# Kernel optimization log

Measured on AMD Instinct MI355X. Metric: run time of the kernel, lower is better.

## Reference

```python
import jax, jax.numpy as jnp
from jax import lax
import numpy as np

VOCAB = 50000
EMBED = 300
H = 128
NUM_CLASS = 2
B, L = 4, 512


def _lstm(x, Wih, Whh, b):
    # x: (B, L, D) -> hidden sequence (B, L, H); PyTorch gate order i,f,g,o
    Bn = x.shape[0]
    h0 = jnp.zeros((Bn, H), dtype=x.dtype)
    c0 = jnp.zeros((Bn, H), dtype=x.dtype)

    def step(carry, xt):
        h, c = carry
        g = xt @ Wih + h @ Whh + b  # (B, 4H)
        i, f, gg, o = jnp.split(g, 4, axis=-1)
        i = jax.nn.sigmoid(i)
        f = jax.nn.sigmoid(f)
        gg = jnp.tanh(gg)
        o = jax.nn.sigmoid(o)
        c = f * c + i * gg
        h = o * jnp.tanh(c)
        return (h, c), h

    _, hs = lax.scan(step, (h0, c0), jnp.swapaxes(x, 0, 1))
    return jnp.swapaxes(hs, 0, 1)


def setup_inputs() -> dict:
    key = jax.random.key(0)
    ks = jax.random.split(key, 12)
    s = lambda fan_in: 1.0 / np.sqrt(fan_in)
    inp = {
        "question_content": jax.random.randint(ks[0], (B, L), 0, VOCAB, dtype=jnp.int32),
        "answer_content": jax.random.randint(ks[1], (B, L), 0, VOCAB, dtype=jnp.int32),
        "embed_table": jax.random.normal(ks[2], (VOCAB, EMBED), dtype=jnp.float32) * 0.1,
        "W_ih": jax.random.uniform(ks[3], (EMBED, 4 * H), jnp.float32, -s(H), s(H)),
        "W_hh": jax.random.uniform(ks[4], (H, 4 * H), jnp.float32, -s(H), s(H)),
        "b_lstm": jax.random.uniform(ks[5], (4 * H,), jnp.float32, -s(H), s(H)),
        "Wa": jax.random.uniform(ks[6], (2 * H, H), jnp.float32, -s(2 * H), s(2 * H)),
        "ba": jnp.zeros((H,), jnp.float32),
        "Wq": jax.random.uniform(ks[7], (2 * H, 1), jnp.float32, -s(2 * H), s(2 * H)),
        "bq": jnp.zeros((1,), jnp.float32),
        "Wans": jax.random.uniform(ks[8], (2 * H, 1), jnp.float32, -s(2 * H), s(2 * H)),
        "bans": jnp.zeros((1,), jnp.float32),
        "Wlast": jax.random.uniform(ks[9], (2 * H, NUM_CLASS), jnp.float32, -s(2 * H), s(2 * H)),
        "blast": jnp.zeros((NUM_CLASS,), jnp.float32),
    }
    return inp


def reference(question_content, answer_content, embed_table, W_ih, W_hh, b_lstm,
              Wa, ba, Wq, bq, Wans, bans, Wlast, blast):
    q_emb = embed_table[question_content]  # (B, Lq, EMBED)
    a_emb = embed_table[answer_content]    # (B, La, EMBED)
    q_lstm = _lstm(q_emb, W_ih, W_hh, b_lstm)  # (B, Lq, H)
    a_lstm = _lstm(a_emb, W_ih, W_hh, b_lstm)  # (B, La, H)

    # A = tanh(Wa @ cat(q_expand, a_expand) + ba); split Wa to avoid the concat copy
    Wa_q, Wa_a = Wa[:H], Wa[H:]
    proj_q = q_lstm @ Wa_q              # (B, Lq, H)
    proj_a = a_lstm @ Wa_a              # (B, La, H)
    A = jnp.tanh(proj_q[:, :, None, :] + proj_a[:, None, :, :] + ba)  # (B, Lq, La, H)

    r_q = jnp.max(A, axis=1)  # max over question positions -> (B, La, H)
    r_a = jnp.max(A, axis=2)  # max over answer positions   -> (B, Lq, H)

    cat_q = jnp.concatenate([q_lstm, r_q], axis=-1)  # (B, L, 2H) (Lq == La)
    cat_a = jnp.concatenate([a_lstm, r_a], axis=-1)
    alpha_q = jax.nn.softmax(cat_q @ Wq + bq, axis=-2)    # (B, L, 1)
    alpha_a = jax.nn.softmax(cat_a @ Wans + bans, axis=-2)

    feature_q = jnp.sum(alpha_q * r_q, axis=-2)  # (B, H)
    feature_a = jnp.sum(alpha_a * r_a, axis=-2)  # (B, H)
    feature_last = jnp.concatenate([feature_q, feature_a], axis=-1)  # (B, 2H)

    score = jax.nn.log_softmax(feature_last @ Wlast + blast, axis=-1)
    predict = jnp.argmax(score, axis=-1)
    return score, predict
```

## Files before the change

### kernel.cpp

```cpp
#include <hip/hip_runtime.h>
#include <hip/hip_bf16.h>

#define EMBED 300
#define HD    128
#define LLEN  512
#define G4    512

#define OFF_LSTM 2097152
#define OFF_PROJ 2621440
#define OFF_MX   3145728

typedef _Float16 half8 __attribute__((ext_vector_type(8)));
typedef float    f32x4 __attribute__((ext_vector_type(4)));

__device__ __forceinline__ float fsig(float x) {
    return __fdividef(1.f, 1.f + __expf(-x));
}
__device__ __forceinline__ float ftanh(float x) {
    return 1.f - __fdividef(2.f, __expf(2.f * x) + 1.f);
}

__global__ __launch_bounds__(256) void k1_gemm(
    const int* __restrict__ qc, const int* __restrict__ ac,
    const float* __restrict__ emb, const float* __restrict__ wih,
    const float* __restrict__ bl, float* __restrict__ preg)
{
    __shared__ float As[32][65];
    __shared__ float Bs[32][64];
    const int m0 = blockIdx.x * 64;
    const int n0 = blockIdx.y * 64;
    const int tid = threadIdx.x;
    const int tx = tid & 15, ty = tid >> 4;
    float acc[4][4] = {};

    for (int k0 = 0; k0 < 300; k0 += 32) {
        #pragma unroll
        for (int i = 0; i < 8; ++i) {
            int e = tid + i * 256;
            int m = e >> 5, kk = e & 31;
            int row = m0 + m;
            int c = row >> 11, b = (row >> 9) & 3, t = row & 511;
            int tok = (c == 0 ? qc : ac)[b * LLEN + t];
            int k = k0 + kk;
            As[kk][m] = (k < 300) ? emb[(size_t)tok * EMBED + k] : 0.f;
        }
        #pragma unroll
        for (int i = 0; i < 8; ++i) {
            int e = tid + i * 256;
            int kk = e >> 6, n = e & 63;
            int k = k0 + kk;
            Bs[kk][n] = (k < 300) ? wih[k * G4 + n0 + n] : 0.f;
        }
        __syncthreads();
        #pragma unroll
        for (int kk = 0; kk < 32; ++kk) {
            float a[4], bv[4];
            #pragma unroll
            for (int i = 0; i < 4; ++i) a[i] = As[kk][ty * 4 + i];
            #pragma unroll
            for (int j = 0; j < 4; ++j) bv[j] = Bs[kk][tx * 4 + j];
            #pragma unroll
            for (int i = 0; i < 4; ++i)
                #pragma unroll
                for (int j = 0; j < 4; ++j)
                    acc[i][j] += a[i] * bv[j];
        }
        __syncthreads();
    }
    #pragma unroll
    for (int i = 0; i < 4; ++i) {
        int row = m0 + ty * 4 + i;
        #pragma unroll
        for (int j = 0; j < 4; ++j) {
            int n = n0 + tx * 4 + j;
            preg[(size_t)row * G4 + n] = acc[i][j] + bl[n];
        }
    }
}

__global__ __launch_bounds__(512, 1) void k2_lstm_mfma(
    const float* __restrict__ whh, const float* __restrict__ preg,
    const float* __restrict__ wa,
    float* __restrict__ lstm, float* __restrict__ proj, float* __restrict__ mx)
{
    const int seq = blockIdx.x;
    const int tid = threadIdx.x;
    const int w  = tid >> 6;
    const int l  = tid & 63;
    const int li = l & 15;
    const int g  = l >> 4;

    __shared__ __align__(16) _Float16 hist[32 * 136];

    half8 afrag[4][4];
    #pragma unroll
    for (int s = 0; s < 4; ++s) {
        const int mg = s * 128 + w * 16 + li;
        #pragma unroll
        for (int kt = 0; kt < 4; ++kt) {
            half8 v;
            #pragma unroll
            for (int e = 0; e < 8; ++e)
                v[e] = (_Float16)whh[(kt * 32 + g * 8 + e) * G4 + mg];
            afrag[kt][s] = v;
        }
    }
    const int s_side = seq >> 2;
    half8 afragW[4];
    #pragma unroll
    for (int kt = 0; kt < 4; ++kt) {
        half8 v;
        #pragma unroll
        for (int e = 0; e < 8; ++e)
            v[e] = (_Float16)wa[(s_side * 128 + kt * 32 + g * 8 + e) * 128 + (w * 16 + li)];
        afragW[kt] = v;
    }

    for (int i = tid; i < 32 * 68; i += 512) ((unsigned*)hist)[i] = 0u;

    const f32x4* pg4 = (const f32x4*)(preg + (size_t)seq * LLEN * G4);
    const int pgo = w * 4 + g;
    const int r   = li & 3;
    const int unit = w * 16 + g * 4 + r;
    const bool wlane = li < 4;
    float* outp = lstm + (size_t)seq * LLEN * HD + unit;
    float cst = 0.f;
    float pmr0 = -1e30f, pmr1 = -1e30f, pmr2 = -1e30f, pmr3 = -1e30f;

    f32x4 pgA[4], pgB[4];
    #pragma unroll
    for (int s = 0; s < 4; ++s) pgA[s] = pg4[0 * 128 + s * 32 + pgo];
    #pragma unroll
    for (int s = 0; s < 4; ++s) pgB[s] = pg4[1 * 128 + s * 32 + pgo];

    __syncthreads();

#define LSTM_STEP(T, PGV, RDS, WRS)                                            \
    {                                                                          \
        half8 bfrag[4];                                                        \
        _Pragma("unroll")                                                      \
        for (int kt = 0; kt < 4; ++kt)                                         \
            bfrag[kt] = *(const half8*)(hist + (RDS) * 136 + kt * 32 + g * 8); \
        f32x4 a0 = PGV[0], a1 = PGV[1], a2 = PGV[2], a3 = PGV[3];              \
        {                                                                      \
            int tp = (T) + 2; if (tp > 511) tp = 511;                          \
            _Pragma("unroll")                                                  \
            for (int s = 0; s < 4; ++s) PGV[s] = pg4[tp * 128 + s * 32 + pgo]; \
        }                                                                      \
        _Pragma("unroll")                                                      \
        for (int kt = 0; kt < 4; ++kt) {                                       \
            a0 = __builtin_amdgcn_mfma_f32_16x16x32_f16(afrag[kt][0], bfrag[kt], a0, 0, 0, 0); \
            a1 = __builtin_amdgcn_mfma_f32_16x16x32_f16(afrag[kt][1], bfrag[kt], a1, 0, 0, 0); \
            a2 = __builtin_amdgcn_mfma_f32_16x16x32_f16(afrag[kt][2], bfrag[kt], a2, 0, 0, 0); \
            a3 = __builtin_amdgcn_mfma_f32_16x16x32_f16(afrag[kt][3], bfrag[kt], a3, 0, 0, 0); \
        }                                                                      \
        float xi = (r == 0) ? a0[0] : (r == 1) ? a0[1] : (r == 2) ? a0[2] : a0[3]; \
        float xf = (r == 0) ? a1[0] : (r == 1) ? a1[1] : (r == 2) ? a1[2] : a1[3]; \
        float xg = (r == 0) ? a2[0] : (r == 1) ? a2[1] : (r == 2) ? a2[2] : a2[3]; \
        float xo = (r == 0) ? a3[0] : (r == 1) ? a3[1] : (r == 2) ? a3[2] : a3[3]; \
        float i_ = fsig(xi), f_ = fsig(xf), g_ = ftanh(xg), o_ = fsig(xo);     \
        cst = f_ * cst + i_ * g_;                                              \
        float h = o_ * ftanh(cst);                                             \
        if (wlane) {                                                           \
            outp[(size_t)(T) * HD] = h;                                        \
            hist[(WRS) * 136 + unit] = (_Float16)h;                            \
        }                                                                      \
        asm volatile("s_waitcnt lgkmcnt(0)" ::: "memory");                     \
        __builtin_amdgcn_sched_barrier(0);                                     \
        __builtin_amdgcn_s_barrier();                                          \
        __builtin_amdgcn_sched_barrier(0);                                     \
    }

#define PROJ_BATCH(P, TBASE)                                                   \
    {                                                                          \
        const _Float16* hb = hist + ((P) * 16 + li) * 136 + g * 8;             \
        half8 bb0 = *(const half8*)(hb + 0 * 32);                              \
        half8 bb1 = *(const half8*)(hb + 1 * 32);                              \
        half8 bb2 = *(const half8*)(hb + 2 * 32);                              \
        half8 bb3 = *(const half8*)(hb + 3 * 32);                              \
        f32x4 pa = {0.f, 0.f, 0.f, 0.f};                                       \
        pa = __builtin_amdgcn_mfma_f32_16x16x32_f16(afragW[0], bb0, pa, 0, 0, 0); \
        pa = __builtin_amdgcn_mfma_f32_16x16x32_f16(afragW[1], bb1, pa, 0, 0, 0); \
        pa = __builtin_amdgcn_mfma_f32_16x16x32_f16(afragW[2], bb2, pa, 0, 0, 0); \
        pa = __builtin_amdgcn_mfma_f32_16x16x32_f16(afragW[3], bb3, pa, 0, 0, 0); \
        float* pp = proj + (size_t)seq * LLEN * HD                             \
                  + (size_t)((TBASE) + li) * HD + w * 16 + g * 4;              \
        *(f32x4*)pp = pa;                                                      \
        pmr0 = fmaxf(pmr0, pa[0]);                                             \
        pmr1 = fmaxf(pmr1, pa[1]);                                             \
        pmr2 = fmaxf(pmr2, pa[2]);                                             \
        pmr3 = fmaxf(pmr3, pa[3]);                                             \
    }

    #pragma unroll 1
    for (int tto = 0; tto < 16; ++tto) {
        const int tb = tto * 32;
        #pragma unroll
        for (int u = 0; u < 16; ++u) {
            const int t0 = tb + u * 2;
            LSTM_STEP(t0,     pgA, (2 * u + 31) & 31, 2 * u);
            LSTM_STEP(t0 + 1, pgB, 2 * u, 2 * u + 1);
            if (u == 7)  PROJ_BATCH(0, tb);
            if (u == 15) PROJ_BATCH(1, tb + 16);
        }
    }
#undef LSTM_STEP
#undef PROJ_BATCH

    #pragma unroll
    for (int m = 1; m <= 8; m <<= 1) {
        pmr0 = fmaxf(pmr0, __shfl_xor(pmr0, m, 64));
        pmr1 = fmaxf(pmr1, __shfl_xor(pmr1, m, 64));
        pmr2 = fmaxf(pmr2, __shfl_xor(pmr2, m, 64));
        pmr3 = fmaxf(pmr3, __shfl_xor(pmr3, m, 64));
    }
    if (li == 0) {
        mx[seq * HD + w * 16 + g * 4 + 0] = pmr0;
        mx[seq * HD + w * 16 + g * 4 + 1] = pmr1;
        mx[seq * HD + w * 16 + g * 4 + 2] = pmr2;
        mx[seq * HD + w * 16 + g * 4 + 3] = pmr3;
    }
}

__global__ __launch_bounds__(512) void k45a_attn(
    const float* __restrict__ lstm, const float* __restrict__ proj,
    const float* __restrict__ mx, const float* __restrict__ ba,
    const float* __restrict__ wq, const float* __restrict__ wans,
    float* __restrict__ pn, float* __restrict__ pd)
{
    const int bid = blockIdx.x;
    const int chunk = bid & 3, sb = bid >> 2;
    const int s = sb >> 2, b = sb & 3;
    const int tid = threadIdx.x;
    const int wave = tid >> 6, lane = tid & 63;

    __shared__ float nred[8][128];
    __shared__ float dred[8];

    const float* wv = (s == 0) ? wq : wans;
    const float* lb = lstm + (size_t)sb * LLEN * HD;
    const float* po = proj + (size_t)((1 - s) * 4 + b) * LLEN * HD;

    const float mb1 = mx[sb * HD + lane] + ba[lane];
    const float mb2 = mx[sb * HD + lane + 64] + ba[lane + 64];
    const float wv1a = wv[lane], wv1b = wv[lane + 64];
    const float wv2a = wv[128 + lane], wv2b = wv[192 + lane];

    float n1 = 0.f, n2 = 0.f, den = 0.f;
    #pragma unroll 4
    for (int jj = 0; jj < 16; ++jj) {
        const int j = chunk * 128 + wave + jj * 8;
        float L1 = lb[(size_t)j * HD + lane];
        float L2 = lb[(size_t)j * HD + lane + 64];
        float P1 = po[(size_t)j * HD + lane];
        float P2 = po[(size_t)j * HD + lane + 64];
        float r1 = ftanh(mb1 + P1), r2 = ftanh(mb2 + P2);
        float sc = L1 * wv1a + L2 * wv1b + r1 * wv2a + r2 * wv2b;
        #pragma unroll
        for (int o = 32; o; o >>= 1) sc += __shfl_xor(sc, o, 64);
        float e = __expf(sc);
        den += e;
        n1 += e * r1;
        n2 += e * r2;
    }
    nred[wave][lane] = n1;
    nred[wave][lane + 64] = n2;
    if (lane == 0) dred[wave] = den;
    __syncthreads();

    if (tid < 128) {
        float s8 = 0.f;
        #pragma unroll
        for (int i = 0; i < 8; ++i) s8 += nred[i][tid];
        pn[bid * 128 + tid] = s8;
    }
    if (tid == 128) {
        float dd = 0.f;
        #pragma unroll
        for (int i = 0; i < 8; ++i) dd += dred[i];
        pd[bid] = dd;
    }
}

__global__ __launch_bounds__(256) void k45b_final(
    const float* __restrict__ pn, const float* __restrict__ pd,
    const float* __restrict__ wlast, const float* __restrict__ blast,
    float* __restrict__ outp)
{
    const int b = blockIdx.x;
    const int tid = threadIdx.x;
    __shared__ float feats[2][128];
    __shared__ float cls[256];

    {
        const int ss = tid >> 7, h = tid & 127;
        const int base = (ss * 4 + b) * 4;
        float num = pn[(base + 0) * 128 + h] + pn[(base + 1) * 128 + h]
                  + pn[(base + 2) * 128 + h] + pn[(base + 3) * 128 + h];
        float dd  = pd[base + 0] + pd[base + 1] + pd[base + 2] + pd[base + 3];
        feats[ss][h] = num / dd;
    }
    __syncthreads();

    if (tid < 128) {
        float f0 = feats[0][tid], f1 = feats[1][tid];
        cls[tid]       = f0 * wlast[tid * 2 + 0] + f1 * wlast[(128 + tid) * 2 + 0];
        cls[128 + tid] = f0 * wlast[tid * 2 + 1] + f1 * wlast[(128 + tid) * 2 + 1];
    }
    __syncthreads();
    if (tid < 64) {
        float a0 = cls[tid] + cls[tid + 64];
        float a1 = cls[128 + tid] + cls[192 + tid];
        #pragma unroll
        for (int o = 32; o; o >>= 1) {
            a0 += __shfl_down(a0, o, 64);
            a1 += __shfl_down(a1, o, 64);
        }
        if (tid == 0) {
            float l0 = blast[0] + a0, l1 = blast[1] + a1;
            float mxl = fmaxf(l0, l1);
            float lse = mxl + logf(__expf(l0 - mxl) + __expf(l1 - mxl));
            outp[b * 2 + 0] = l0 - lse;
            outp[b * 2 + 1] = l1 - lse;
            outp[8 + b]     = (l1 > l0) ? 1.f : 0.f;
        }
    }
}

extern "C" void kernel_launch(void* const* d_in, const int* in_sizes, int n_in,
                              void* d_out, int out_size, void* d_ws, size_t ws_size,
                              hipStream_t stream)
{
    const int*   qc    = (const int*)d_in[0];
    const int*   ac    = (const int*)d_in[1];
    const float* emb   = (const float*)d_in[2];
    const float* wih   = (const float*)d_in[3];
    const float* whh   = (const float*)d_in[4];
    const float* bl    = (const float*)d_in[5];
    const float* wa    = (const float*)d_in[6];
    const float* ba    = (const float*)d_in[7];
    const float* wq    = (const float*)d_in[8];
    const float* wans  = (const float*)d_in[10];
    const float* wlast = (const float*)d_in[12];
    const float* blast = (const float*)d_in[13];

    float* ws   = (float*)d_ws;
    float* preg = ws;
    float* lstm = ws + OFF_LSTM;
    float* proj = ws + OFF_PROJ;
    float* mx   = ws + OFF_MX;
    float* pn   = ws;
    float* pd   = ws + 4096;

    k1_gemm<<<dim3(64, 8), 256, 0, stream>>>(qc, ac, emb, wih, bl, preg);
    k2_lstm_mfma<<<8, 512, 0, stream>>>(whh, preg, wa, lstm, proj, mx);
    k45a_attn<<<32, 512, 0, stream>>>(lstm, proj, mx, ba, wq, wans, pn, pd);
    k45b_final<<<4, 256, 0, stream>>>(pn, pd, wlast, blast, (float*)d_out);
}
```

Baseline: 381.6 us.

## Split LSTM recurrent matmul K across two wave groups with LDS reduction

Doubles the LSTM block to 1024 threads and has the upper eight waves compute half of the K-reduction of h@Whh, passing partial sums through shared memory to the lower waves. The lower waves add the partials and apply the gate nonlinearities. This shortens the dependent MFMA chain per timestep. It costs an extra LDS store/load and a second block-wide barrier on every step, and the time loop is no longer fully unrolled.

```diff
diff --git a/kernel.cpp b/kernel.cpp
--- a/kernel.cpp
+++ b/kernel.cpp
@@ -78,31 +78,35 @@
     }
 }
 
-__global__ __launch_bounds__(512, 1) void k2_lstm_mfma(
+__global__ __launch_bounds__(1024, 1) void k2_lstm_mfma(
     const float* __restrict__ whh, const float* __restrict__ preg,
     const float* __restrict__ wa,
     float* __restrict__ lstm, float* __restrict__ proj, float* __restrict__ mx)
 {
     const int seq = blockIdx.x;
     const int tid = threadIdx.x;
-    const int w  = tid >> 6;
+    const int w   = tid >> 6;
+    const int wl  = w & 7;
+    const bool lower = w < 8;
     const int l  = tid & 63;
     const int li = l & 15;
     const int g  = l >> 4;
+    const int ktb = lower ? 0 : 2;
 
     __shared__ __align__(16) _Float16 hist[32 * 136];
-
-    half8 afrag[4][4];
+    __shared__ __align__(16) f32x4 red[4 * 8 * 64];
+
+    half8 afrag[2][4];
     #pragma unroll
     for (int s = 0; s < 4; ++s) {
-        const int mg = s * 128 + w * 16 + li;
-        #pragma unroll
-        for (int kt = 0; kt < 4; ++kt) {
+        const int mg = s * 128 + wl * 16 + li;
+        #pragma unroll
+        for (int ktl = 0; ktl < 2; ++ktl) {
             half8 v;
             #pragma unroll
             for (int e = 0; e < 8; ++e)
-                v[e] = (_Float16)whh[(kt * 32 + g * 8 + e) * G4 + mg];
-            afrag[kt][s] = v;
+                v[e] = (_Float16)whh[((ktb + ktl) * 32 + g * 8 + e) * G4 + mg];
+            afrag[ktl][s] = v;
         }
     }
     const int s_side = seq >> 2;
@@ -112,67 +116,84 @@
         half8 v;
         #pragma unroll
         for (int e = 0; e < 8; ++e)
-            v[e] = (_Float16)wa[(s_side * 128 + kt * 32 + g * 8 + e) * 128 + (w * 16 + li)];
+            v[e] = (_Float16)wa[(s_side * 128 + kt * 32 + g * 8 + e) * 128 + (wl * 16 + li)];
         afragW[kt] = v;
     }
 
-    for (int i = tid; i < 32 * 68; i += 512) ((unsigned*)hist)[i] = 0u;
+    for (int i = tid; i < 32 * 68; i += 1024) ((unsigned*)hist)[i] = 0u;
 
     const f32x4* pg4 = (const f32x4*)(preg + (size_t)seq * LLEN * G4);
-    const int pgo = w * 4 + g;
+    const int pgo = wl * 4 + g;
     const int r   = li & 3;
-    const int unit = w * 16 + g * 4 + r;
+    const int unit = wl * 16 + g * 4 + r;
     const bool wlane = li < 4;
     float* outp = lstm + (size_t)seq * LLEN * HD + unit;
     float cst = 0.f;
     float pmr0 = -1e30f, pmr1 = -1e30f, pmr2 = -1e30f, pmr3 = -1e30f;
 
-    f32x4 pgA[4], pgB[4];
-    #pragma unroll
-    for (int s = 0; s < 4; ++s) pgA[s] = pg4[0 * 128 + s * 32 + pgo];
-    #pragma unroll
-    for (int s = 0; s < 4; ++s) pgB[s] = pg4[1 * 128 + s * 32 + pgo];
+    f32x4 pgA[4] = {}, pgB[4] = {};
+    if (lower) {
+        #pragma unroll
+        for (int s = 0; s < 4; ++s) pgA[s] = pg4[0 * 128 + s * 32 + pgo];
+        #pragma unroll
+        for (int s = 0; s < 4; ++s) pgB[s] = pg4[1 * 128 + s * 32 + pgo];
+    }
 
     __syncthreads();
 
 #define LSTM_STEP(T, PGV, RDS, WRS)                                            \
     {                                                                          \
-        half8 bfrag[4];                                                        \
-        _Pragma("unroll")                                                      \
-        for (int kt = 0; kt < 4; ++kt)                                         \
-            bfrag[kt] = *(const half8*)(hist + (RDS) * 136 + kt * 32 + g * 8); \
-        f32x4 a0 = PGV[0], a1 = PGV[1], a2 = PGV[2], a3 = PGV[3];              \
-        {                                                                      \
+        const _Float16* hp = hist + (RDS) * 136 + ktb * 32 + g * 8;            \
+        half8 bfrag0 = *(const half8*)(hp);                                    \
+        half8 bfrag1 = *(const half8*)(hp + 32);                               \
+        f32x4 a0, a1, a2, a3;                                                  \
+        if (lower) {                                                           \
+            a0 = PGV[0]; a1 = PGV[1]; a2 = PGV[2]; a3 = PGV[3];                \
             int tp = (T) + 2; if (tp > 511) tp = 511;                          \
             _Pragma("unroll")                                                  \
             for (int s = 0; s < 4; ++s) PGV[s] = pg4[tp * 128 + s * 32 + pgo]; \
+        } else {                                                               \
+            a0 = (f32x4){0.f,0.f,0.f,0.f}; a1 = a0; a2 = a0; a3 = a0;          \
         }                                                                      \
-        _Pragma("unroll")                                                      \
-        for (int kt = 0; kt < 4; ++kt) {                                       \
-            a0 = __builtin_amdgcn_mfma_f32_16x16x32_f16(afrag[kt][0], bfrag[kt], a0, 0, 0, 0); \
-            a1 = __builtin_amdgcn_mfma_f32_16x16x32_f16(afrag[kt][1], bfrag[kt], a1, 0, 0, 0); \
-            a2 = __builtin_amdgcn_mfma_f32_16x16x32_f16(afrag[kt][2], bfrag[kt], a2, 0, 0, 0); \
-            a3 = __builtin_amdgcn_mfma_f32_16x16x32_f16(afrag[kt][3], bfrag[kt], a3, 0, 0, 0); \
-        }                                                                      \
-        float xi = (r == 0) ? a0[0] : (r == 1) ? a0[1] : (r == 2) ? a0[2] : a0[3]; \
-        float xf = (r == 0) ? a1[0] : (r == 1) ? a1[1] : (r == 2) ? a1[2] : a1[3]; \
-        float xg = (r == 0) ? a2[0] : (r == 1) ? a2[1] : (r == 2) ? a2[2] : a2[3]; \
-        float xo = (r == 0) ? a3[0] : (r == 1) ? a3[1] : (r == 2) ? a3[2] : a3[3]; \
-        float i_ = fsig(xi), f_ = fsig(xf), g_ = ftanh(xg), o_ = fsig(xo);     \
-        cst = f_ * cst + i_ * g_;                                              \
-        float h = o_ * ftanh(cst);                                             \
-        if (wlane) {                                                           \
-            outp[(size_t)(T) * HD] = h;                                        \
-            hist[(WRS) * 136 + unit] = (_Float16)h;                            \
+        a0 = __builtin_amdgcn_mfma_f32_16x16x32_f16(afrag[0][0], bfrag0, a0, 0, 0, 0); \
+        a1 = __builtin_amdgcn_mfma_f32_16x16x32_f16(afrag[0][1], bfrag0, a1, 0, 0, 0); \
+        a2 = __builtin_amdgcn_mfma_f32_16x16x32_f16(afrag[0][2], bfrag0, a2, 0, 0, 0); \
+        a3 = __builtin_amdgcn_mfma_f32_16x16x32_f16(afrag[0][3], bfrag0, a3, 0, 0, 0); \
+        a0 = __builtin_amdgcn_mfma_f32_16x16x32_f16(afrag[1][0], bfrag1, a0, 0, 0, 0); \
+        a1 = __builtin_amdgcn_mfma_f32_16x16x32_f16(afrag[1][1], bfrag1, a1, 0, 0, 0); \
+        a2 = __builtin_amdgcn_mfma_f32_16x16x32_f16(afrag[1][2], bfrag1, a2, 0, 0, 0); \
+        a3 = __builtin_amdgcn_mfma_f32_16x16x32_f16(afrag[1][3], bfrag1, a3, 0, 0, 0); \
+        if (!lower) {                                                          \
+            f32x4* rp = red + wl * 64 + l;                                     \
+            rp[0] = a0; rp[512] = a1; rp[1024] = a2; rp[1536] = a3;            \
         }                                                                      \
         asm volatile("s_waitcnt lgkmcnt(0)" ::: "memory");                     \
         __builtin_amdgcn_sched_barrier(0);                                     \
         __builtin_amdgcn_s_barrier();                                          \
         __builtin_amdgcn_sched_barrier(0);                                     \
+        if (lower) {                                                           \
+            const f32x4* rp = red + wl * 64 + l;                               \
+            a0 += rp[0]; a1 += rp[512]; a2 += rp[1024]; a3 += rp[1536];        \
+            float xi = (r == 0) ? a0[0] : (r == 1) ? a0[1] : (r == 2) ? a0[2] : a0[3]; \
+            float xf = (r == 0) ? a1[0] : (r == 1) ? a1[1] : (r == 2) ? a1[2] : a1[3]; \
+            float xg = (r == 0) ? a2[0] : (r == 1) ? a2[1] : (r == 2) ? a2[2] : a2[3]; \
+            float xo = (r == 0) ? a3[0] : (r == 1) ? a3[1] : (r == 2) ? a3[2] : a3[3]; \
+            float i_ = fsig(xi), f_ = fsig(xf), g_ = ftanh(xg), o_ = fsig(xo); \
+            cst = f_ * cst + i_ * g_;                                          \
+            float h = o_ * ftanh(cst);                                         \
+            if (wlane) {                                                       \
+                outp[(size_t)(T) * HD] = h;                                    \
+                hist[(WRS) * 136 + unit] = (_Float16)h;                        \
+            }                                                                  \
+        }                                                                      \
+        asm volatile("s_waitcnt lgkmcnt(0)" ::: "memory");                     \
+        __builtin_amdgcn_sched_barrier(0);                                     \
+        __builtin_amdgcn_s_barrier();                                          \
+        __builtin_amdgcn_sched_barrier(0);                                     \
     }
 
 #define PROJ_BATCH(P, TBASE)                                                   \
-    {                                                                          \
+    if (lower) {                                                               \
         const _Float16* hb = hist + ((P) * 16 + li) * 136 + g * 8;             \
         half8 bb0 = *(const half8*)(hb + 0 * 32);                              \
         half8 bb1 = *(const half8*)(hb + 1 * 32);                              \
@@ -184,7 +205,7 @@
         pa = __builtin_amdgcn_mfma_f32_16x16x32_f16(afragW[2], bb2, pa, 0, 0, 0); \
         pa = __builtin_amdgcn_mfma_f32_16x16x32_f16(afragW[3], bb3, pa, 0, 0, 0); \
         float* pp = proj + (size_t)seq * LLEN * HD                             \
-                  + (size_t)((TBASE) + li) * HD + w * 16 + g * 4;              \
+                  + (size_t)((TBASE) + li) * HD + wl * 16 + g * 4;             \
         *(f32x4*)pp = pa;                                                      \
         pmr0 = fmaxf(pmr0, pa[0]);                                             \
         pmr1 = fmaxf(pmr1, pa[1]);                                             \
@@ -193,32 +214,33 @@
     }
 
     #pragma unroll 1
-    for (int tto = 0; tto < 16; ++tto) {
-        const int tb = tto * 32;
-        #pragma unroll
-        for (int u = 0; u < 16; ++u) {
-            const int t0 = tb + u * 2;
-            LSTM_STEP(t0,     pgA, (2 * u + 31) & 31, 2 * u);
-            LSTM_STEP(t0 + 1, pgB, 2 * u, 2 * u + 1);
-            if (u == 7)  PROJ_BATCH(0, tb);
-            if (u == 15) PROJ_BATCH(1, tb + 16);
+    for (int tt = 0; tt < 256; ++tt) {
+        const int t0 = tt * 2;
+        const int s0 = t0 & 31;
+        LSTM_STEP(t0,     pgA, (s0 + 31) & 31, s0);
+        LSTM_STEP(t0 + 1, pgB, s0, s0 + 1);
+        if ((tt & 7) == 7) {
+            const int p = (tt >> 3) & 1;
+            PROJ_BATCH(p, t0 - 14);
         }
     }
 #undef LSTM_STEP
 #undef PROJ_BATCH
 
-    #pragma unroll
-    for (int m = 1; m <= 8; m <<= 1) {
-        pmr0 = fmaxf(pmr0, __shfl_xor(pmr0, m, 64));
-        pmr1 = fmaxf(pmr1, __shfl_xor(pmr1, m, 64));
-        pmr2 = fmaxf(pmr2, __shfl_xor(pmr2, m, 64));
-        pmr3 = fmaxf(pmr3, __shfl_xor(pmr3, m, 64));
-    }
-    if (li == 0) {
-        mx[seq * HD + w * 16 + g * 4 + 0] = pmr0;
-        mx[seq * HD + w * 16 + g * 4 + 1] = pmr1;
-        mx[seq * HD + w * 16 + g * 4 + 2] = pmr2;
-        mx[seq * HD + w * 16 + g * 4 + 3] = pmr3;
+    if (lower) {
+        #pragma unroll
+        for (int m = 1; m <= 8; m <<= 1) {
+            pmr0 = fmaxf(pmr0, __shfl_xor(pmr0, m, 64));
+            pmr1 = fmaxf(pmr1, __shfl_xor(pmr1, m, 64));
+            pmr2 = fmaxf(pmr2, __shfl_xor(pmr2, m, 64));
+            pmr3 = fmaxf(pmr3, __shfl_xor(pmr3, m, 64));
+        }
+        if (li == 0) {
+            mx[seq * HD + wl * 16 + g * 4 + 0] = pmr0;
+            mx[seq * HD + wl * 16 + g * 4 + 1] = pmr1;
+            mx[seq * HD + wl * 16 + g * 4 + 2] = pmr2;
+            mx[seq * HD + wl * 16 + g * 4 + 3] = pmr3;
+        }
     }
 }
 
@@ -353,7 +375,7 @@
     float* pd   = ws + 4096;
 
     k1_gemm<<<dim3(64, 8), 256, 0, stream>>>(qc, ac, emb, wih, bl, preg);
-    k2_lstm_mfma<<<8, 512, 0, stream>>>(whh, preg, wa, lstm, proj, mx);
+    k2_lstm_mfma<<<8, 1024, 0, stream>>>(whh, preg, wa, lstm, proj, mx);
     k45a_attn<<<32, 512, 0, stream>>>(lstm, proj, mx, ba, wq, wans, pn, pd);
     k45b_final<<<4, 256, 0, stream>>>(pn, pd, wlast, blast, (float*)d_out);
 }
```

Result: slower. 667.1 us (+74.8%).

## Pack two LSTM sequences per 1024-thread block and reroll time loop

Applied to the files above, without the earlier changes.

The recurrent LSTM kernel now runs two sequences per workgroup of 1024 threads across 4 blocks, with a separate shared-memory history buffer for each half. The fully unrolled 32-step inner loop becomes a rolled loop with computed history slot indices and conditional projection batches. The aim is to halve the number of CUs used and let two recurrences interleave on the same SIMDs to hide latency. In exchange, every per-step barrier now synchronises both sequences, and the 1024-thread launch bound cuts the per-thread register budget, which risks spilling the resident weight fragments.

```diff
diff --git a/kernel.cpp b/kernel.cpp
--- a/kernel.cpp
+++ b/kernel.cpp
@@ -78,19 +78,21 @@
     }
 }
 
-__global__ __launch_bounds__(512, 1) void k2_lstm_mfma(
+__global__ __launch_bounds__(1024, 1) void k2_lstm_mfma(
     const float* __restrict__ whh, const float* __restrict__ preg,
     const float* __restrict__ wa,
     float* __restrict__ lstm, float* __restrict__ proj, float* __restrict__ mx)
 {
-    const int seq = blockIdx.x;
-    const int tid = threadIdx.x;
+    const int half = threadIdx.x >> 9;
+    const int seq  = blockIdx.x * 2 + half;
+    const int tid  = threadIdx.x & 511;
     const int w  = tid >> 6;
     const int l  = tid & 63;
     const int li = l & 15;
     const int g  = l >> 4;
 
-    __shared__ __align__(16) _Float16 hist[32 * 136];
+    __shared__ __align__(16) _Float16 hist[2][32 * 136];
+    _Float16* hst = hist[half];
 
     half8 afrag[4][4];
     #pragma unroll
@@ -116,7 +118,7 @@
         afragW[kt] = v;
     }
 
-    for (int i = tid; i < 32 * 68; i += 512) ((unsigned*)hist)[i] = 0u;
+    for (int i = tid; i < 32 * 68; i += 512) ((unsigned*)hst)[i] = 0u;
 
     const f32x4* pg4 = (const f32x4*)(preg + (size_t)seq * LLEN * G4);
     const int pgo = w * 4 + g;
@@ -140,7 +142,7 @@
         half8 bfrag[4];                                                        \
         _Pragma("unroll")                                                      \
         for (int kt = 0; kt < 4; ++kt)                                         \
-            bfrag[kt] = *(const half8*)(hist + (RDS) * 136 + kt * 32 + g * 8); \
+            bfrag[kt] = *(const half8*)(hst + (RDS) * 136 + kt * 32 + g * 8);  \
         f32x4 a0 = PGV[0], a1 = PGV[1], a2 = PGV[2], a3 = PGV[3];              \
         {                                                                      \
             int tp = (T) + 2; if (tp > 511) tp = 511;                          \
@@ -163,7 +165,7 @@
         float h = o_ * ftanh(cst);                                             \
         if (wlane) {                                                           \
             outp[(size_t)(T) * HD] = h;                                        \
-            hist[(WRS) * 136 + unit] = (_Float16)h;                            \
+            hst[(WRS) * 136 + unit] = (_Float16)h;                             \
         }                                                                      \
         asm volatile("s_waitcnt lgkmcnt(0)" ::: "memory");                     \
         __builtin_amdgcn_sched_barrier(0);                                     \
@@ -173,7 +175,7 @@
 
 #define PROJ_BATCH(P, TBASE)                                                   \
     {                                                                          \
-        const _Float16* hb = hist + ((P) * 16 + li) * 136 + g * 8;             \
+        const _Float16* hb = hst + ((P) * 16 + li) * 136 + g * 8;              \
         half8 bb0 = *(const half8*)(hb + 0 * 32);                              \
         half8 bb1 = *(const half8*)(hb + 1 * 32);                              \
         half8 bb2 = *(const half8*)(hb + 2 * 32);                              \
@@ -193,15 +195,14 @@
     }
 
     #pragma unroll 1
-    for (int tto = 0; tto < 16; ++tto) {
-        const int tb = tto * 32;
-        #pragma unroll
-        for (int u = 0; u < 16; ++u) {
-            const int t0 = tb + u * 2;
-            LSTM_STEP(t0,     pgA, (2 * u + 31) & 31, 2 * u);
-            LSTM_STEP(t0 + 1, pgB, 2 * u, 2 * u + 1);
-            if (u == 7)  PROJ_BATCH(0, tb);
-            if (u == 15) PROJ_BATCH(1, tb + 16);
+    for (int tt = 0; tt < 256; ++tt) {
+        const int t0 = tt * 2;
+        const int s0 = t0 & 31;
+        LSTM_STEP(t0,     pgA, (s0 + 31) & 31, s0);
+        LSTM_STEP(t0 + 1, pgB, s0, s0 + 1);
+        if ((tt & 7) == 7) {
+            const int p = (tt >> 3) & 1;
+            PROJ_BATCH(p, t0 - 14);
         }
     }
 #undef LSTM_STEP
@@ -353,7 +354,7 @@
     float* pd   = ws + 4096;
 
     k1_gemm<<<dim3(64, 8), 256, 0, stream>>>(qc, ac, emb, wih, bl, preg);
-    k2_lstm_mfma<<<8, 512, 0, stream>>>(whh, preg, wa, lstm, proj, mx);
+    k2_lstm_mfma<<<4, 1024, 0, stream>>>(whh, preg, wa, lstm, proj, mx);
     k45a_attn<<<32, 512, 0, stream>>>(lstm, proj, mx, ba, wq, wans, pn, pd);
     k45b_final<<<4, 256, 0, stream>>>(pn, pd, wlast, blast, (float*)d_out);
 }
```

Result: slower. 820.0 us (+114.9%).
